# Kernel optimization log

Measured on AMD Instinct MI355X. Metric: run time of the kernel, lower is better.

The kernel has to match this reference:

```python
import jax, jax.numpy as jnp
import numpy as np

B, S, D, H = 2, 2048, 2048, 16
HD = D // H            # 128
BLK = 16               # sparsity block size
LOCAL = 4              # num_local_blocks
GLOBAL = 1             # num_global_blocks
ROPE_THETA = 10000.0


def _fixed_layout(num_blocks: int) -> np.ndarray:
    """DeepSpeed FixedSparsityConfig block layout (unidirectional,
    different_layout_per_head=False, num_different_global_patterns=1,
    horizontal_global_attention=False)."""
    layout = np.zeros((num_blocks, num_blocks), dtype=bool)
    # local windows of LOCAL blocks, causal at block granularity inside window
    for w in range(0, num_blocks, LOCAL):
        end = min(w + LOCAL, num_blocks)
        for row in range(w, end):
            layout[row, w:row + 1] = True
    # vertical global columns: last GLOBAL block(s) of each window
    first = LOCAL - GLOBAL  # head % num_different_global_patterns == 0
    stop = num_blocks - (num_blocks % LOCAL)
    for i in range(first, stop, LOCAL):
        layout[i:, i:i + GLOBAL] = True  # unidirectional: rows >= i
    return layout

_LAYOUT = _fixed_layout(S // BLK)  # [num_blocks, num_blocks] bool, static


def _rope(t, cos, sin):
    # t: [B, S, H, HD]; pairs are adjacent (llama complex view)
    tr = t.reshape(B, S, H, HD // 2, 2)
    a, b = tr[..., 0], tr[..., 1]
    c = cos[None, :, None, :]
    s = sin[None, :, None, :]
    out = jnp.stack([a * c - b * s, a * s + b * c], axis=-1)
    return out.reshape(B, S, H, HD)


def setup_inputs() -> dict:
    key = jax.random.key(0)
    kx, kq, kk, kv, ko = jax.random.split(key, 5)
    x = jax.random.normal(kx, (B, S, D), dtype=jnp.float32)
    wscale = 1.0 / np.sqrt(D)
    wq = jax.random.normal(kq, (D, D), dtype=jnp.float32) * wscale
    wk = jax.random.normal(kk, (D, D), dtype=jnp.float32) * wscale
    wv = jax.random.normal(kv, (D, D), dtype=jnp.float32) * wscale
    wo = jax.random.normal(ko, (D, D), dtype=jnp.float32) * wscale
    # rotary tables (freqs_cis split into real/imag parts)
    freqs = 1.0 / (ROPE_THETA ** (np.arange(0, HD, 2, dtype=np.float32) / HD))
    angles = np.arange(S, dtype=np.float32)[:, None] * freqs[None, :]  # [S, HD//2]
    cos = jnp.asarray(np.cos(angles), dtype=jnp.float32)
    sin = jnp.asarray(np.sin(angles), dtype=jnp.float32)
    return {"x": x, "cos": cos, "sin": sin, "wq": wq, "wk": wk, "wv": wv, "wo": wo}


def reference(x, cos, sin, wq, wk, wv, wo):
    xq = (x @ wq).reshape(B, S, H, HD)
    xk = (x @ wk).reshape(B, S, H, HD)
    xv = (x @ wv).reshape(B, S, H, HD)
    xq = _rope(xq, cos, sin)
    xk = _rope(xk, cos, sin)
    # module casts q/k/v to fp16 before the sparse kernel; emulate precision
    xq = xq.astype(jnp.float16).astype(jnp.float32)
    xk = xk.astype(jnp.float16).astype(jnp.float32)
    xv = xv.astype(jnp.float16).astype(jnp.float32)
    q = jnp.transpose(xq, (0, 2, 1, 3))  # [B, H, S, HD]
    k = jnp.transpose(xk, (0, 2, 1, 3))
    v = jnp.transpose(xv, (0, 2, 1, 3))
    scale = 1.0 / np.sqrt(HD)
    scores = jnp.einsum('bhqd,bhkd->bhqk', q, k) * scale
    # block-granularity sparsity mask (DeepSpeed masks only at block level)
    blk = jnp.arange(S) // BLK
    mask = jnp.asarray(_LAYOUT)[blk[:, None], blk[None, :]]  # [S, S] bool
    scores = jnp.where(mask[None, None], scores, -jnp.inf)
    probs = jax.nn.softmax(scores, axis=-1)
    out = jnp.einsum('bhqk,bhkd->bhqd', probs, v)  # [B, H, S, HD]
    out = jnp.transpose(out, (0, 2, 1, 3)).reshape(B, S, D)
    return out @ wo
```

## Files before the change

kernel.cpp:

```cpp
#include <hip/hip_runtime.h>

#define B_ 2
#define S_ 2048
#define D_ 2048
#define H_ 16
#define HD_ 128

typedef _Float16 fp16x2 __attribute__((ext_vector_type(2)));
typedef _Float16 fp16x4 __attribute__((ext_vector_type(4)));
typedef _Float16 fp16x8 __attribute__((ext_vector_type(8)));
typedef float f32x4 __attribute__((ext_vector_type(4)));

__device__ __forceinline__ void gl_lds16(const _Float16* g, _Float16* l) {
  __builtin_amdgcn_global_load_lds((const __attribute__((address_space(1))) void*)g,
                                   (__attribute__((address_space(3))) void*)l, 16, 0, 0);
}

__global__ __launch_bounds__(256) void k_cast(const float* __restrict__ in,
                                              _Float16* __restrict__ out, int n4) {
  int i = blockIdx.x * 256 + threadIdx.x;
  if (i >= n4) return;
  f32x4 v = ((const f32x4*)in)[i];
  fp16x4 h = {(_Float16)v[0], (_Float16)v[1], (_Float16)v[2], (_Float16)v[3]};
  ((fp16x4*)out)[i] = h;
}

__global__ __launch_bounds__(256) void k_trw4(const float* __restrict__ w0,
                                              const float* __restrict__ w1,
                                              const float* __restrict__ w2,
                                              const float* __restrict__ w3,
                                              _Float16* __restrict__ o0,
                                              _Float16* __restrict__ o1,
                                              _Float16* __restrict__ o2,
                                              _Float16* __restrict__ o3) {
  __shared__ float tile[64][65];
  const float* w = (blockIdx.z == 0) ? w0 : (blockIdx.z == 1) ? w1 : (blockIdx.z == 2) ? w2 : w3;
  _Float16* wt = (blockIdx.z == 0) ? o0 : (blockIdx.z == 1) ? o1 : (blockIdx.z == 2) ? o2 : o3;
  int k0 = blockIdx.y * 64, n0 = blockIdx.x * 64;
  int t = threadIdx.x;
  int r = t >> 2, c0 = (t & 3) * 16;
  const float* ip = w + (size_t)(k0 + r) * D_ + n0 + c0;
#pragma unroll
  for (int j = 0; j < 16; j += 4) {
    f32x4 v = *(const f32x4*)(ip + j);
    tile[r][c0 + j] = v[0]; tile[r][c0 + j + 1] = v[1];
    tile[r][c0 + j + 2] = v[2]; tile[r][c0 + j + 3] = v[3];
  }
  __syncthreads();
  _Float16* op = wt + (size_t)(n0 + r) * D_ + k0 + c0;
#pragma unroll
  for (int j = 0; j < 16; j += 8) {
    fp16x8 v;
#pragma unroll
    for (int q = 0; q < 8; ++q) v[q] = (_Float16)tile[c0 + j + q][r];
    *(fp16x8*)(op + j) = v;
  }
}

template <int MODE>
__global__ __launch_bounds__(512) void k_gemm256(const _Float16* __restrict__ A,
                                                 const _Float16* __restrict__ BT,
                                                 const float* __restrict__ cosT,
                                                 const float* __restrict__ sinT,
                                                 _Float16* __restrict__ Qo,
                                                 _Float16* __restrict__ Ko,
                                                 _Float16* __restrict__ Vo,
                                                 float* __restrict__ Cf) {
  __shared__ __align__(16) _Float16 smem[49152];
  const int tid = threadIdx.x;
  const int w = tid >> 6, lane = tid & 63;
  const int l15 = lane & 15, lg = lane >> 4;
  const int NPX = (MODE == 0) ? 6 : 2;
  const int bid = blockIdx.x;
  const int xcd = bid & 7, j = bid >> 3;
  const int m0 = (j / NPX) * 256;
  const int n0 = (xcd * NPX + j % NPX) * 128;
  const int wm = (w >> 1) * 64;
  const int wn = (w & 1) * 64;
  const int lr = lane >> 3, lc = lane & 7;
  const int scol = (lc ^ lr) << 3;
  const _Float16* Asrc = A + (size_t)(m0 + w * 8 + lr) * 2048 + scol;
  const _Float16* Bsrc = BT + (size_t)(n0 + w * 8 + lr) * 2048 + scol;
  _Float16* dstA = smem + w * 512;
  _Float16* dstB = smem + 32768 + w * 512;

  auto stageA = [&](int stg, int u, int k0) {
    gl_lds16(Asrc + (size_t)u * 64 * 2048 + k0, dstA + stg * 16384 + u * 4096);
  };
  auto stageB = [&](int stg, int u, int k0) {
    gl_lds16(Bsrc + (size_t)u * 64 * 2048 + k0, dstB + stg * 8192 + u * 4096);
  };

  f32x4 acc[4][4] = {};

#pragma unroll
  for (int u = 0; u < 4; ++u) stageA(0, u, 0);
  stageB(0, 0, 0); stageB(0, 1, 0);

  for (int t = 0; t < 32; ++t) {
    const int cur = t & 1, stg = cur ^ 1;
    if (t + 1 < 32) {
      const int k1 = (t + 1) * 64;
#pragma unroll
      for (int u = 0; u < 4; ++u) stageA(stg, u, k1);
      stageB(stg, 0, k1); stageB(stg, 1, k1);
      asm volatile("s_waitcnt vmcnt(6)" ::: "memory");
    } else {
      asm volatile("s_waitcnt vmcnt(0)" ::: "memory");
    }
    __builtin_amdgcn_s_barrier();

    fp16x8 af[4][2], bf[4][2];
#pragma unroll
    for (int mi = 0; mi < 4; ++mi)
#pragma unroll
      for (int ks = 0; ks < 2; ++ks) {
        const int row = wm + mi * 16 + l15;
        af[mi][ks] = *(const fp16x8*)(smem + cur * 16384 + (row >> 6) * 4096 +
                                      (row & 63) * 64 + ((ks * 32 + lg * 8) ^ ((l15 & 7) * 8)));
      }
#pragma unroll
    for (int ni = 0; ni < 4; ++ni)
#pragma unroll
      for (int ks = 0; ks < 2; ++ks) {
        const int row = wn + ni * 16 + l15;
        bf[ni][ks] = *(const fp16x8*)(smem + 32768 + cur * 8192 + (row >> 6) * 4096 +
                                      (row & 63) * 64 + ((ks * 32 + lg * 8) ^ ((l15 & 7) * 8)));
      }
    __builtin_amdgcn_s_setprio(1);
#pragma unroll
    for (int mi = 0; mi < 4; ++mi)
#pragma unroll
      for (int ni = 0; ni < 4; ++ni)
#pragma unroll
        for (int ks = 0; ks < 2; ++ks)
          acc[mi][ni] = __builtin_amdgcn_mfma_f32_16x16x32_f16(af[mi][ks], bf[ni][ks],
                                                               acc[mi][ni], 0, 0, 0);
    __builtin_amdgcn_s_setprio(0);
    __builtin_amdgcn_s_barrier();
  }

  if (MODE == 0) {
    const int region = n0 >> 11;
    if (region < 2) {
      _Float16* Out = (region == 0) ? Qo : Ko;
#pragma unroll
      for (int mi = 0; mi < 4; ++mi)
#pragma unroll
        for (int ni = 0; ni < 4; ++ni) {
          const int col = n0 + wn + 16 * ni + l15;
          const int d = col & 127;
          const int h = (col >> 7) & 15;
          const int dp = d >> 1;
          const bool odd = d & 1;
#pragma unroll
          for (int i = 0; i < 4; ++i) {
            const int row = m0 + wm + 16 * mi + 4 * lg + i;
            const int b = row >> 11, sl = row & 2047;
            const float self = acc[mi][ni][i];
            const float partner = __shfl_xor(self, 1);
            const float c = cosT[sl * 64 + dp], sn = sinT[sl * 64 + dp];
            const float val = odd ? (partner * sn + self * c) : (self * c - partner * sn);
            Out[(((size_t)b * H_ + h) * S_ + sl) * HD_ + d] = (_Float16)val;
          }
        }
    } else {
#pragma unroll
      for (int mi = 0; mi < 4; ++mi)
#pragma unroll
        for (int ni = 0; ni < 4; ++ni) {
          const int col = n0 + wn + 16 * ni + l15;
          const int d = col & 127;
          const int h = (col >> 7) & 15;
          const int row0 = m0 + wm + 16 * mi + 4 * lg;
          const int b = row0 >> 11, sl0 = row0 & 2047;
          const int kb = sl0 >> 4, kin = sl0 & 15;
          fp16x4 v4;
#pragma unroll
          for (int i = 0; i < 4; ++i) v4[i] = (_Float16)acc[mi][ni][i];
          *(fp16x4*)(Vo + ((((size_t)b * H_ + h) * 128 + kb) * 128 + d) * 16 + kin) = v4;
        }
    }
  } else {
#pragma unroll
    for (int mi = 0; mi < 4; ++mi)
#pragma unroll
      for (int ni = 0; ni < 4; ++ni) {
        const size_t row = m0 + wm + 16 * mi + 4 * lg;
        const size_t col = n0 + wn + 16 * ni + l15;
#pragma unroll
        for (int i = 0; i < 4; ++i)
          Cf[(row + i) * 2048 + col] = acc[mi][ni][i];
      }
  }
}

__global__ __launch_bounds__(256) void k_attn(const _Float16* __restrict__ Q,
                                              const _Float16* __restrict__ K,
                                              const _Float16* __restrict__ Vb,
                                              _Float16* __restrict__ Oa) {
  __shared__ __align__(16) _Float16 sK[2][2][2048];
  __shared__ __align__(16) _Float16 sV[2][2][2048];
  const int p = blockIdx.x;
  const int qgA = 31 - p, qgB = p;
  const int hh = blockIdx.y, b = blockIdx.z;
  const int t = threadIdx.x;
  const int w = t >> 6, lane = t & 63;
  const int l15 = lane & 15, lg = lane >> 4, g4 = lg * 4;
  const size_t bh = (size_t)b * H_ + hh;
  const float scale = 0.08838834764831845f;

  const int qbA = 4 * qgA + w, qbB = 4 * qgB + w;
  const int LA = qgA + 4, LB = qgB + 4;
  const int nchA = (LA + 1) >> 1, nchB = (LB + 1) >> 1;
  const int total = nchA + nchB;

  const _Float16* QpA = Q + (bh * S_ + (size_t)qbA * 16 + l15) * HD_ + lg * 8;
  const _Float16* QpB = Q + (bh * S_ + (size_t)qbB * 16 + l15) * HD_ + lg * 8;
  fp16x8 qfA[4], qfB[4];
#pragma unroll
  for (int dd = 0; dd < 4; ++dd) {
    qfA[dd] = *(const fp16x8*)(QpA + dd * 32);
    qfB[dd] = *(const fp16x8*)(QpB + dd * 32);
  }
  f32x4 o[8] = {};
  float mrun = -3.0e38f, lsum = 0.f;

  const int sr = t >> 4, sc = t & 15;
  const int ksrc_off = sr * 128 + (sc ^ (sr & 7)) * 8;
  const _Float16* Kb_g = K + bh * S_ * HD_;
  const _Float16* Vb_g = Vb + bh * (size_t)(128 * 2048);

  auto kbof = [&](int qg, int idx) { return idx < qg ? 4 * idx + 3 : 3 * qg + idx; };
  auto chunk_kbs = [&](int ci, int& kb0, int& kb1) {
    int qg, cil;
    if (ci < nchA) { qg = qgA; cil = ci; } else { qg = qgB; cil = ci - nchA; }
    const int L = qg + 4;
    const int i0 = 2 * cil, i1 = i0 + 1;
    kb0 = kbof(qg, i0);
    kb1 = (i1 < L) ? kbof(qg, i1) : kb0;
  };
  auto stage = [&](int buf, int ci) {
    int kb0, kb1;
    chunk_kbs(ci, kb0, kb1);
    gl_lds16(Kb_g + (size_t)kb0 * 2048 + ksrc_off, &sK[buf][0][w * 512]);
    gl_lds16(Kb_g + (size_t)kb1 * 2048 + ksrc_off, &sK[buf][1][w * 512]);
    gl_lds16(Vb_g + (size_t)kb0 * 2048 + t * 8, &sV[buf][0][w * 512]);
    gl_lds16(Vb_g + (size_t)kb1 * 2048 + t * 8, &sV[buf][1][w * 512]);
  };
  auto flush = [&](int qb) {
    const float inv = 1.f / lsum;
    f32x4 li;
#pragma unroll
    for (int i = 0; i < 4; ++i) li[i] = __shfl(inv, g4 + i);
    _Float16* Op = Oa + ((size_t)b * S_ + (size_t)qb * 16 + g4) * D_ + (size_t)hh * HD_ + l15;
#pragma unroll
    for (int ni = 0; ni < 8; ++ni)
#pragma unroll
      for (int i = 0; i < 4; ++i)
        Op[(size_t)i * D_ + 16 * ni] = (_Float16)(o[ni][i] * li[i]);
  };

  stage(0, 0);

  for (int ci = 0; ci < total; ++ci) {
    const int cur = ci & 1;
    if (ci == nchA) {
      flush(qbA);
#pragma unroll
      for (int ni = 0; ni < 8; ++ni) o[ni] = f32x4{0.f, 0.f, 0.f, 0.f};
      mrun = -3.0e38f;
      lsum = 0.f;
    }
    if (ci + 1 < total) {
      stage(cur ^ 1, ci + 1);
      asm volatile("s_waitcnt vmcnt(4)" ::: "memory");
    } else {
      asm volatile("s_waitcnt vmcnt(0)" ::: "memory");
    }
    __builtin_amdgcn_s_barrier();

    const bool inA = ci < nchA;
    const int qg = inA ? qgA : qgB;
    const int qb = inA ? qbA : qbB;
    const int cil = inA ? ci : ci - nchA;
    const int L = qg + 4;
    int kb0, kb1;
    chunk_kbs(ci, kb0, kb1);
    const bool v0 = kb0 <= qb;
    const bool v1 = (2 * cil + 1 < L) && (kb1 <= qb);
    f32x4 st[2];
    const float in0 = v0 ? 0.f : -1.0e30f, in1 = v1 ? 0.f : -1.0e30f;
    st[0] = f32x4{in0, in0, in0, in0};
    st[1] = f32x4{in1, in1, in1, in1};

    const char* kl = (const char*)&sK[cur][0][0];
    const int krow = l15 * 256;
#pragma unroll
    for (int dd = 0; dd < 4; ++dd) {
      const int co = ((dd * 4 + lg) ^ (l15 & 7)) * 16;
      fp16x8 k0 = *(const fp16x8*)(kl + krow + co);
      fp16x8 k1 = *(const fp16x8*)(kl + 4096 + krow + co);
      const fp16x8 qf = inA ? qfA[dd] : qfB[dd];
      st[0] = __builtin_amdgcn_mfma_f32_16x16x32_f16(k0, qf, st[0], 0, 0, 0);
      st[1] = __builtin_amdgcn_mfma_f32_16x16x32_f16(k1, qf, st[1], 0, 0, 0);
    }
    float bm = -3.0e38f;
#pragma unroll
    for (int j = 0; j < 2; ++j)
#pragma unroll
      for (int i = 0; i < 4; ++i) {
        st[j][i] *= scale;
        bm = fmaxf(bm, st[j][i]);
      }
    bm = fmaxf(bm, __shfl_xor(bm, 16));
    bm = fmaxf(bm, __shfl_xor(bm, 32));
    const float mnew = fmaxf(mrun, bm);
    const float corr = __expf(mrun - mnew);
    float pr[2][4];
    float ps = 0.f;
#pragma unroll
    for (int j = 0; j < 2; ++j)
#pragma unroll
      for (int i = 0; i < 4; ++i) {
        pr[j][i] = __expf(st[j][i] - mnew);
        ps += pr[j][i];
      }
    ps += __shfl_xor(ps, 16);
    ps += __shfl_xor(ps, 32);
    lsum = lsum * corr + ps;
    mrun = mnew;
    f32x4 c4;
#pragma unroll
    for (int i = 0; i < 4; ++i) c4[i] = __shfl(corr, g4 + i);
#pragma unroll
    for (int ni = 0; ni < 8; ++ni) {
      o[ni][0] *= c4[0]; o[ni][1] *= c4[1]; o[ni][2] *= c4[2]; o[ni][3] *= c4[3];
    }
    fp16x4 ph0 = {(_Float16)pr[0][0], (_Float16)pr[0][1], (_Float16)pr[0][2], (_Float16)pr[0][3]};
    fp16x4 ph1 = {(_Float16)pr[1][0], (_Float16)pr[1][1], (_Float16)pr[1][2], (_Float16)pr[1][3]};
    const char* vl = (const char*)&sV[cur][0][0];
#pragma unroll
    for (int ni = 0; ni < 8; ++ni) {
      const int vo = (16 * ni + l15) * 32 + g4 * 2;
      fp16x4 vv0 = *(const fp16x4*)(vl + vo);
      fp16x4 vv1 = *(const fp16x4*)(vl + 4096 + vo);
      o[ni] = __builtin_amdgcn_mfma_f32_16x16x16f16(ph0, vv0, o[ni], 0, 0, 0);
      o[ni] = __builtin_amdgcn_mfma_f32_16x16x16f16(ph1, vv1, o[ni], 0, 0, 0);
    }
    __builtin_amdgcn_s_barrier();
  }

  flush(qbB);
}

extern "C" void kernel_launch(void* const* d_in, const int* in_sizes, int n_in,
                              void* d_out, int out_size, void* d_ws, size_t ws_size,
                              hipStream_t stream) {
  const float* x = (const float*)d_in[0];
  const float* cosT = (const float*)d_in[1];
  const float* sinT = (const float*)d_in[2];
  const float* wq = (const float*)d_in[3];
  const float* wk = (const float*)d_in[4];
  const float* wv = (const float*)d_in[5];
  const float* wo = (const float*)d_in[6];
  float* out = (float*)d_out;
  char* ws = (char*)d_ws;

  _Float16* x16 = (_Float16*)(ws);
  _Float16* wtq = (_Float16*)(ws + (16ull << 20));
  _Float16* wtk = (_Float16*)(ws + (24ull << 20));
  _Float16* wtv = (_Float16*)(ws + (32ull << 20));
  _Float16* wto = (_Float16*)(ws + (40ull << 20));
  _Float16* Q16 = (_Float16*)(ws + (48ull << 20));
  _Float16* K16 = (_Float16*)(ws + (64ull << 20));
  _Float16* Vb16 = (_Float16*)(ws + (80ull << 20));

  k_cast<<<8192, 256, 0, stream>>>(x, x16, (B_ * S_ * D_) / 4);
  k_trw4<<<dim3(32, 32, 4), 256, 0, stream>>>(wq, wk, wv, wo, wtq, wtk, wtv, wto);

  k_gemm256<0><<<768, 512, 0, stream>>>(x16, wtq, cosT, sinT, Q16, K16, Vb16, nullptr);

  _Float16* attn16 = x16;
  k_attn<<<dim3(16, H_, B_), 256, 0, stream>>>(Q16, K16, Vb16, attn16);

  k_gemm256<1><<<256, 512, 0, stream>>>(attn16, wto, nullptr, nullptr, nullptr, nullptr,
                                        nullptr, out);
}
```

Baseline: 221.7 us.

## Triple-buffer GEMM LDS stages and interleave prefetch with half-K MFMA steps

Raises the 256x128 GEMM's LDS buffering from two stages to three, so global-to-LDS loads for step t+2 are issued while step t computes. Each K step is split into two half steps, with the prefetch loads spread across them and barriers placed between LDS reads and MFMAs. LDS row offsets and swizzles are also hoisted out of the loop. LDS use grows to about 144 KB per block, and the extra barriers per iteration could offset the deeper overlap.

```diff
diff --git a/kernel.cpp b/kernel.cpp
--- a/kernel.cpp
+++ b/kernel.cpp
@@ -66,7 +66,7 @@
                                                  _Float16* __restrict__ Ko,
                                                  _Float16* __restrict__ Vo,
                                                  float* __restrict__ Cf) {
-  __shared__ __align__(16) _Float16 smem[49152];
+  __shared__ __align__(16) _Float16 smem[73728];
   const int tid = threadIdx.x;
   const int w = tid >> 6, lane = tid & 63;
   const int l15 = lane & 15, lg = lane >> 4;
@@ -82,7 +82,7 @@
   const _Float16* Asrc = A + (size_t)(m0 + w * 8 + lr) * 2048 + scol;
   const _Float16* Bsrc = BT + (size_t)(n0 + w * 8 + lr) * 2048 + scol;
   _Float16* dstA = smem + w * 512;
-  _Float16* dstB = smem + 32768 + w * 512;
+  _Float16* dstB = smem + 49152 + w * 512;
 
   auto stageA = [&](int stg, int u, int k0) {
     gl_lds16(Asrc + (size_t)u * 64 * 2048 + k0, dstA + stg * 16384 + u * 4096);
@@ -91,53 +91,65 @@
     gl_lds16(Bsrc + (size_t)u * 64 * 2048 + k0, dstB + stg * 8192 + u * 4096);
   };
 
+  int aoff[4], boff[4];
+#pragma unroll
+  for (int mi = 0; mi < 4; ++mi) {
+    const int row = wm + mi * 16 + l15;
+    aoff[mi] = (row >> 6) * 4096 + (row & 63) * 64;
+  }
+#pragma unroll
+  for (int ni = 0; ni < 4; ++ni) {
+    const int row = wn + ni * 16 + l15;
+    boff[ni] = (row >> 6) * 4096 + (row & 63) * 64;
+  }
+  const int swz[2] = {(lg * 8) ^ ((l15 & 7) * 8), (32 + lg * 8) ^ ((l15 & 7) * 8)};
+
   f32x4 acc[4][4] = {};
 
 #pragma unroll
   for (int u = 0; u < 4; ++u) stageA(0, u, 0);
   stageB(0, 0, 0); stageB(0, 1, 0);
+#pragma unroll
+  for (int u = 0; u < 4; ++u) stageA(1, u, 64);
+  stageB(1, 0, 64); stageB(1, 1, 64);
+  asm volatile("s_waitcnt vmcnt(6)" ::: "memory");
+  __builtin_amdgcn_s_barrier();
 
   for (int t = 0; t < 32; ++t) {
-    const int cur = t & 1, stg = cur ^ 1;
-    if (t + 1 < 32) {
-      const int k1 = (t + 1) * 64;
-#pragma unroll
-      for (int u = 0; u < 4; ++u) stageA(stg, u, k1);
-      stageB(stg, 0, k1); stageB(stg, 1, k1);
-      asm volatile("s_waitcnt vmcnt(6)" ::: "memory");
-    } else {
-      asm volatile("s_waitcnt vmcnt(0)" ::: "memory");
-    }
-    __builtin_amdgcn_s_barrier();
-
-    fp16x8 af[4][2], bf[4][2];
-#pragma unroll
-    for (int mi = 0; mi < 4; ++mi)
-#pragma unroll
-      for (int ks = 0; ks < 2; ++ks) {
-        const int row = wm + mi * 16 + l15;
-        af[mi][ks] = *(const fp16x8*)(smem + cur * 16384 + (row >> 6) * 4096 +
-                                      (row & 63) * 64 + ((ks * 32 + lg * 8) ^ ((l15 & 7) * 8)));
+    const int cur = t % 3;
+    const bool pf = (t + 2) < 32;
+    const int spf = (t + 2) % 3, kpf = (t + 2) * 64;
+    const _Float16* sA = smem + cur * 16384;
+    const _Float16* sB = smem + 49152 + cur * 8192;
+#pragma unroll
+    for (int ks = 0; ks < 2; ++ks) {
+      fp16x8 af[4], bf[4];
+#pragma unroll
+      for (int mi = 0; mi < 4; ++mi) af[mi] = *(const fp16x8*)(sA + aoff[mi] + swz[ks]);
+#pragma unroll
+      for (int ni = 0; ni < 4; ++ni) bf[ni] = *(const fp16x8*)(sB + boff[ni] + swz[ks]);
+      if (ks == 0) {
+        if (pf) { stageA(spf, 0, kpf); stageA(spf, 1, kpf); stageA(spf, 2, kpf); }
+      } else {
+        if (pf) {
+          stageA(spf, 3, kpf); stageB(spf, 0, kpf); stageB(spf, 1, kpf);
+          asm volatile("s_waitcnt vmcnt(6)" ::: "memory");
+        } else {
+          asm volatile("s_waitcnt vmcnt(0)" ::: "memory");
+        }
       }
-#pragma unroll
-    for (int ni = 0; ni < 4; ++ni)
-#pragma unroll
-      for (int ks = 0; ks < 2; ++ks) {
-        const int row = wn + ni * 16 + l15;
-        bf[ni][ks] = *(const fp16x8*)(smem + 32768 + cur * 8192 + (row >> 6) * 4096 +
-                                      (row & 63) * 64 + ((ks * 32 + lg * 8) ^ ((l15 & 7) * 8)));
-      }
-    __builtin_amdgcn_s_setprio(1);
-#pragma unroll
-    for (int mi = 0; mi < 4; ++mi)
-#pragma unroll
-      for (int ni = 0; ni < 4; ++ni)
-#pragma unroll
-        for (int ks = 0; ks < 2; ++ks)
-          acc[mi][ni] = __builtin_amdgcn_mfma_f32_16x16x32_f16(af[mi][ks], bf[ni][ks],
+      __builtin_amdgcn_s_barrier();
+      asm volatile("s_waitcnt lgkmcnt(0)" ::: "memory");
+      __builtin_amdgcn_s_setprio(1);
+#pragma unroll
+      for (int mi = 0; mi < 4; ++mi)
+#pragma unroll
+        for (int ni = 0; ni < 4; ++ni)
+          acc[mi][ni] = __builtin_amdgcn_mfma_f32_16x16x32_f16(af[mi], bf[ni],
                                                                acc[mi][ni], 0, 0, 0);
-    __builtin_amdgcn_s_setprio(0);
-    __builtin_amdgcn_s_barrier();
+      __builtin_amdgcn_s_setprio(0);
+      __builtin_amdgcn_s_barrier();
+    }
   }
 
   if (MODE == 0) {
```

Measured after the change: 225.2 us. No clear change (+1.6%).
